# Optimization experiments

Hardware: AMD Instinct MI355X
Metric: run time of the kernel (lower is better)

Reference implementation:

```python
import jax, jax.numpy as jnp
import numpy as np

IN_F = 1024
OUT_F = 1024
DEGREE = 7  # degree+1 = 8 Chebyshev terms


def setup_inputs() -> dict:
    key = jax.random.key(0)
    k1, k2, k3 = jax.random.split(key, 3)
    x = jax.random.normal(k1, (16384, IN_F), dtype=jnp.float32)
    std = 1.0 / (IN_F * (DEGREE + 1))
    cheby_coeffs = jax.random.normal(k2, (OUT_F, IN_F, DEGREE + 1), dtype=jnp.float32) * std
    # xavier_uniform for base_weight [out, in]
    limit = float(np.sqrt(6.0 / (IN_F + OUT_F)))
    base_weight = jax.random.uniform(k3, (OUT_F, IN_F), dtype=jnp.float32, minval=-limit, maxval=limit)
    return {"x": x, "cheby_coeffs": cheby_coeffs, "base_weight": base_weight}


def _cheby_basis(x_norm, degree):
    terms = [jnp.ones_like(x_norm), x_norm]
    for _ in range(2, degree + 1):
        terms.append(2.0 * x_norm * terms[-1] - terms[-2])
    return jnp.stack(terms, axis=-1)  # [b, i, d+1]


def reference(x, cheby_coeffs, base_weight):
    x_norm = jnp.tanh(x)
    basis = _cheby_basis(x_norm, DEGREE)               # [b, i, d]
    kan_out = jnp.einsum('bid,oid->bo', basis, cheby_coeffs)
    base_out = x @ base_weight.T                        # F.linear
    return kan_out + base_out
```

## Files before the change

### kernel.cpp

```cpp
#include <hip/hip_runtime.h>
#include <hip/hip_bf16.h>
#include <stdint.h>

typedef short short8 __attribute__((ext_vector_type(8)));
typedef float f32x16 __attribute__((ext_vector_type(16)));

#define KD 8192
#define NT 128

__device__ __forceinline__ unsigned short bfb(float f) {
    __hip_bfloat16 h = __float2bfloat16(f);
    return __builtin_bit_cast(unsigned short, h);
}

__device__ __forceinline__ short8 cheby8(float xv) {
    float e  = __builtin_amdgcn_exp2f(xv * 2.8853900817779268f);
    float xn = 1.0f - 2.0f * __builtin_amdgcn_rcpf(1.0f + e);
    float x2 = xn + xn;
    float t2 = x2 * xn - 1.0f;
    float t3 = x2 * t2 - xn;
    float t4 = x2 * t3 - t2;
    float t5 = x2 * t4 - t3;
    float t6 = x2 * t5 - t4;
    float t7 = x2 * t6 - t5;
    short8 v;
    v[0] = bfb(xv); v[1] = bfb(xn); v[2] = bfb(t2); v[3] = bfb(t3);
    v[4] = bfb(t4); v[5] = bfb(t5); v[6] = bfb(t6); v[7] = bfb(t7);
    return v;
}

__global__ void prep_w(const float* __restrict__ C, const float* __restrict__ W,
                       unsigned short* __restrict__ Bw) {
    int g = blockIdx.x * 256 + threadIdx.x;
    int o = g >> 10, i = g & 1023;
    const float* src = C + ((size_t)o * 8192 + i * 8);
    float4 v0 = *(const float4*)src;
    float4 v1 = *(const float4*)(src + 4);
    v0.x = W[o * 1024 + i];
    short8 r;
    r[0] = bfb(v0.x); r[1] = bfb(v0.y); r[2] = bfb(v0.z); r[3] = bfb(v0.w);
    r[4] = bfb(v1.x); r[5] = bfb(v1.y); r[6] = bfb(v1.z); r[7] = bfb(v1.w);
    *(short8*)(Bw + (size_t)g * 8) = r;
}

__global__ void prep_bias(const float* __restrict__ C, float* __restrict__ bias) {
    int o = blockIdx.x;
    int tid = threadIdx.x;
    float s = 0.f;
    for (int i = tid; i < 1024; i += 256)
        s += C[(size_t)o * 8192 + (size_t)i * 8];
    #pragma unroll
    for (int off = 32; off > 0; off >>= 1) s += __shfl_down(s, off);
    __shared__ float red[4];
    if ((tid & 63) == 0) red[tid >> 6] = s;
    __syncthreads();
    if (tid == 0) bias[o] = red[0] + red[1] + red[2] + red[3];
}


#define GLDS(NXT_, C_, TT_) \
    __builtin_amdgcn_global_load_lds( \
        (const __attribute__((address_space(1))) unsigned int*)((const char*)Bw + boff[C_] + (size_t)(TT_) * 128), \
        (__attribute__((address_space(3))) unsigned int*)(&Bs[NXT_][(wave * 4 + (C_)) * 8][0]), 16, 0, 0)

#define PHASE(CUR_, KK_) { \
    const int fb_ = (KK_) * 2 + lg;   \
    float xv0_ = Xs[CUR_][fb_][wm + lr]; \
    float xv1_ = Xs[CUR_][fb_][wm + 32 + lr]; \
    float xv2_ = Xs[CUR_][fb_][wm + 64 + lr]; \
    float xv3_ = Xs[CUR_][fb_][wm + 96 + lr]; \
    const int row0_ = wn + lr, row1_ = wn + 32 + lr; \
    short8 b0_ = *(const short8*)((const char*)&Bs[CUR_][0][0] + row0_ * 128 + ((fb_ ^ (row0_ & 7)) * 16)); \
    short8 b1_ = *(const short8*)((const char*)&Bs[CUR_][0][0] + row1_ * 128 + ((fb_ ^ (row1_ & 7)) * 16)); \
    short8 a0_ = cheby8(xv0_); \
    short8 a1_ = cheby8(xv1_); \
    short8 a2_ = cheby8(xv2_); \
    short8 a3_ = cheby8(xv3_); \
    __builtin_amdgcn_s_setprio(1); \
    acc[0][0] = __builtin_amdgcn_mfma_f32_32x32x16_bf16(a0_, b0_, acc[0][0], 0, 0, 0); \
    acc[0][1] = __builtin_amdgcn_mfma_f32_32x32x16_bf16(a0_, b1_, acc[0][1], 0, 0, 0); \
    acc[1][0] = __builtin_amdgcn_mfma_f32_32x32x16_bf16(a1_, b0_, acc[1][0], 0, 0, 0); \
    acc[1][1] = __builtin_amdgcn_mfma_f32_32x32x16_bf16(a1_, b1_, acc[1][1], 0, 0, 0); \
    acc[2][0] = __builtin_amdgcn_mfma_f32_32x32x16_bf16(a2_, b0_, acc[2][0], 0, 0, 0); \
    acc[2][1] = __builtin_amdgcn_mfma_f32_32x32x16_bf16(a2_, b1_, acc[2][1], 0, 0, 0); \
    acc[3][0] = __builtin_amdgcn_mfma_f32_32x32x16_bf16(a3_, b0_, acc[3][0], 0, 0, 0); \
    acc[3][1] = __builtin_amdgcn_mfma_f32_32x32x16_bf16(a3_, b1_, acc[3][1], 0, 0, 0); \
    __builtin_amdgcn_s_setprio(0); \
}

#define TILE(CUR_, NXT_, T_) { \
    const int tn_ = ((T_) + 1 < NT) ? (T_) + 1 : NT - 1; \
    float4 xr_ = *(const float4*)(xbase + (size_t)tn_ * 8);   \
    GLDS(NXT_, 0, tn_); GLDS(NXT_, 1, tn_); GLDS(NXT_, 2, tn_); GLDS(NXT_, 3, tn_); \
    PHASE(CUR_, 0) \
    PHASE(CUR_, 1) \
    Xs[NXT_][xf + 0][arow] = xr_.x; \
    Xs[NXT_][xf + 1][arow] = xr_.y; \
    Xs[NXT_][xf + 2][arow] = xr_.z; \
    Xs[NXT_][xf + 3][arow] = xr_.w; \
    PHASE(CUR_, 2) \
    PHASE(CUR_, 3) \
    __syncthreads(); \
}

__global__ __launch_bounds__(512, 2)
void cheby_gemm(const float* __restrict__ X, const unsigned short* __restrict__ Bw,
                const float* __restrict__ bias, float* __restrict__ Out) {
    __shared__ unsigned short Bs[2][256][64];
    __shared__ float Xs[2][8][256];

    const int tid  = threadIdx.x;
    const int lane = tid & 63;
    const int wave = tid >> 6;

    int bid = blockIdx.x;
    int lin = (bid & 7) * 32 + (bid >> 3);
    const int m0 = (lin & 63) << 8;
    const int n0 = (lin >> 6) << 8;

    const int wm = (wave >> 2) * 128;
    const int wn = (wave & 3) * 64;
    const int lr = lane & 31;
    const int lg = lane >> 5;

    const int arow = tid >> 1;
    const int xf   = (tid & 1) * 4;
    const float* xbase = X + (size_t)(m0 + arow) * 1024 + xf;

    unsigned int boff[4];
    #pragma unroll
    for (int c = 0; c < 4; ++c) {
        int row   = (wave * 4 + c) * 8 + (lane >> 3);
        int chunk = (lane & 7) ^ (lane >> 3);
        boff[c] = ((unsigned)(n0 + row) * 8192u + (unsigned)chunk * 8u) * 2u;
    }

    f32x16 acc[4][2] = {};

    {
        float4 xr_ = *(const float4*)(xbase);
        GLDS(0, 0, 0); GLDS(0, 1, 0); GLDS(0, 2, 0); GLDS(0, 3, 0);
        Xs[0][xf + 0][arow] = xr_.x;
        Xs[0][xf + 1][arow] = xr_.y;
        Xs[0][xf + 2][arow] = xr_.z;
        Xs[0][xf + 3][arow] = xr_.w;
        __syncthreads();
    }

    for (int t = 0; t < NT; t += 2) {
        TILE(0, 1, t)
        TILE(1, 0, t + 1)
    }

    #pragma unroll
    for (int ni = 0; ni < 2; ++ni) {
        int col = n0 + wn + ni * 32 + lr;
        float bv = bias[col];
        #pragma unroll
        for (int mi = 0; mi < 4; ++mi) {
            #pragma unroll
            for (int r = 0; r < 16; ++r) {
                int row = m0 + wm + mi * 32 + 4 * lg + (r & 3) + 8 * (r >> 2);
                Out[(size_t)row * 1024 + col] = acc[mi][ni][r] + bv;
            }
        }
    }
}

extern "C" void kernel_launch(void* const* d_in, const int* in_sizes, int n_in,
                              void* d_out, int out_size, void* d_ws, size_t ws_size,
                              hipStream_t stream) {
    const float* x = (const float*)d_in[0];
    const float* C = (const float*)d_in[1];
    const float* W = (const float*)d_in[2];
    float* out = (float*)d_out;

    unsigned short* Bw = (unsigned short*)d_ws;
    float* bias = (float*)((char*)d_ws + (size_t)16 * 1024 * 1024);

    prep_w<<<4096, 256, 0, stream>>>(C, W, Bw);
    prep_bias<<<1024, 256, 0, stream>>>(C, bias);
    cheby_gemm<<<256, 512, 0, stream>>>(x, Bw, bias, out);
}
```

Baseline: 321.0 us.

## Reshape wave tile to 64x128 and hand-schedule loads with explicit waitcnts

Each wave now covers 64 rows by 128 columns instead of 128 by 64. That halves how often the Chebyshev basis (exp, rcp, recurrence, bf16 conversions) is recomputed for each x element across waves. The cost is twice as many B-fragment LDS reads per phase. The X global load moves to inline asm, and `__syncthreads` is replaced by explicit `s_waitcnt vmcnt`/`lgkmcnt` plus `s_barrier` with sched_barriers, so global_load_lds of the next tile can overlap the four MFMA phases. The X store to LDS now happens after all phases. The hand-written vmcnt counts risk being wrong if the compiler emits extra memory operations.

```diff
diff --git a/kernel.cpp b/kernel.cpp
--- a/kernel.cpp
+++ b/kernel.cpp
@@ -63,44 +63,54 @@
         (const __attribute__((address_space(1))) unsigned int*)((const char*)Bw + boff[C_] + (size_t)(TT_) * 128), \
         (__attribute__((address_space(3))) unsigned int*)(&Bs[NXT_][(wave * 4 + (C_)) * 8][0]), 16, 0, 0)
 
+#define XLOAD(DST_, TI_) { \
+    const float* ap_ = xbase + (size_t)(TI_) * 8; \
+    asm volatile("global_load_dwordx4 %0, %1, off" : "=&v"(DST_) : "v"(ap_)); }
+
 #define PHASE(CUR_, KK_) { \
-    const int fb_ = (KK_) * 2 + lg;   \
+    const int fb_ = (KK_) * 2 + lg; \
+    const int co_ = (fb_ ^ (lr & 7)) * 16; \
     float xv0_ = Xs[CUR_][fb_][wm + lr]; \
     float xv1_ = Xs[CUR_][fb_][wm + 32 + lr]; \
-    float xv2_ = Xs[CUR_][fb_][wm + 64 + lr]; \
-    float xv3_ = Xs[CUR_][fb_][wm + 96 + lr]; \
-    const int row0_ = wn + lr, row1_ = wn + 32 + lr; \
-    short8 b0_ = *(const short8*)((const char*)&Bs[CUR_][0][0] + row0_ * 128 + ((fb_ ^ (row0_ & 7)) * 16)); \
-    short8 b1_ = *(const short8*)((const char*)&Bs[CUR_][0][0] + row1_ * 128 + ((fb_ ^ (row1_ & 7)) * 16)); \
+    short8 b0_ = *(const short8*)((const char*)&Bs[CUR_][0][0] + (wn +  0 + lr) * 128 + co_); \
+    short8 b1_ = *(const short8*)((const char*)&Bs[CUR_][0][0] + (wn + 32 + lr) * 128 + co_); \
+    short8 b2_ = *(const short8*)((const char*)&Bs[CUR_][0][0] + (wn + 64 + lr) * 128 + co_); \
+    short8 b3_ = *(const short8*)((const char*)&Bs[CUR_][0][0] + (wn + 96 + lr) * 128 + co_); \
     short8 a0_ = cheby8(xv0_); \
     short8 a1_ = cheby8(xv1_); \
-    short8 a2_ = cheby8(xv2_); \
-    short8 a3_ = cheby8(xv3_); \
     __builtin_amdgcn_s_setprio(1); \
     acc[0][0] = __builtin_amdgcn_mfma_f32_32x32x16_bf16(a0_, b0_, acc[0][0], 0, 0, 0); \
     acc[0][1] = __builtin_amdgcn_mfma_f32_32x32x16_bf16(a0_, b1_, acc[0][1], 0, 0, 0); \
+    acc[0][2] = __builtin_amdgcn_mfma_f32_32x32x16_bf16(a0_, b2_, acc[0][2], 0, 0, 0); \
+    acc[0][3] = __builtin_amdgcn_mfma_f32_32x32x16_bf16(a0_, b3_, acc[0][3], 0, 0, 0); \
     acc[1][0] = __builtin_amdgcn_mfma_f32_32x32x16_bf16(a1_, b0_, acc[1][0], 0, 0, 0); \
     acc[1][1] = __builtin_amdgcn_mfma_f32_32x32x16_bf16(a1_, b1_, acc[1][1], 0, 0, 0); \
-    acc[2][0] = __builtin_amdgcn_mfma_f32_32x32x16_bf16(a2_, b0_, acc[2][0], 0, 0, 0); \
-    acc[2][1] = __builtin_amdgcn_mfma_f32_32x32x16_bf16(a2_, b1_, acc[2][1], 0, 0, 0); \
-    acc[3][0] = __builtin_amdgcn_mfma_f32_32x32x16_bf16(a3_, b0_, acc[3][0], 0, 0, 0); \
-    acc[3][1] = __builtin_amdgcn_mfma_f32_32x32x16_bf16(a3_, b1_, acc[3][1], 0, 0, 0); \
+    acc[1][2] = __builtin_amdgcn_mfma_f32_32x32x16_bf16(a1_, b2_, acc[1][2], 0, 0, 0); \
+    acc[1][3] = __builtin_amdgcn_mfma_f32_32x32x16_bf16(a1_, b3_, acc[1][3], 0, 0, 0); \
     __builtin_amdgcn_s_setprio(0); \
 }
 
 #define TILE(CUR_, NXT_, T_) { \
     const int tn_ = ((T_) + 1 < NT) ? (T_) + 1 : NT - 1; \
-    float4 xr_ = *(const float4*)(xbase + (size_t)tn_ * 8);   \
+    float4 xr_; \
+    XLOAD(xr_, tn_) \
     GLDS(NXT_, 0, tn_); GLDS(NXT_, 1, tn_); GLDS(NXT_, 2, tn_); GLDS(NXT_, 3, tn_); \
+    asm volatile("s_waitcnt vmcnt(5)" ::: "memory");  \
+    __builtin_amdgcn_sched_barrier(0); \
+    __builtin_amdgcn_s_barrier(); \
     PHASE(CUR_, 0) \
     PHASE(CUR_, 1) \
+    PHASE(CUR_, 2) \
+    PHASE(CUR_, 3) \
+    asm volatile("s_waitcnt vmcnt(4)" ::: "memory");  \
+    __builtin_amdgcn_sched_barrier(0); \
     Xs[NXT_][xf + 0][arow] = xr_.x; \
     Xs[NXT_][xf + 1][arow] = xr_.y; \
     Xs[NXT_][xf + 2][arow] = xr_.z; \
     Xs[NXT_][xf + 3][arow] = xr_.w; \
-    PHASE(CUR_, 2) \
-    PHASE(CUR_, 3) \
-    __syncthreads(); \
+    asm volatile("s_waitcnt lgkmcnt(0)" ::: "memory"); \
+    __builtin_amdgcn_sched_barrier(0); \
+    __builtin_amdgcn_s_barrier(); \
 }
 
 __global__ __launch_bounds__(512, 2)
@@ -118,8 +128,8 @@
     const int m0 = (lin & 63) << 8;
     const int n0 = (lin >> 6) << 8;
 
-    const int wm = (wave >> 2) * 128;
-    const int wn = (wave & 3) * 64;
+    const int wm = (wave >> 1) * 64;
+    const int wn = (wave & 1) * 128;
     const int lr = lane & 31;
     const int lg = lane >> 5;
 
@@ -135,16 +145,21 @@
         boff[c] = ((unsigned)(n0 + row) * 8192u + (unsigned)chunk * 8u) * 2u;
     }
 
-    f32x16 acc[4][2] = {};
+    f32x16 acc[2][4] = {};
 
     {
-        float4 xr_ = *(const float4*)(xbase);
+        float4 xr_;
+        XLOAD(xr_, 0)
         GLDS(0, 0, 0); GLDS(0, 1, 0); GLDS(0, 2, 0); GLDS(0, 3, 0);
+        asm volatile("s_waitcnt vmcnt(4)" ::: "memory");
+        __builtin_amdgcn_sched_barrier(0);
         Xs[0][xf + 0][arow] = xr_.x;
         Xs[0][xf + 1][arow] = xr_.y;
         Xs[0][xf + 2][arow] = xr_.z;
         Xs[0][xf + 3][arow] = xr_.w;
-        __syncthreads();
+        asm volatile("s_waitcnt lgkmcnt(0)" ::: "memory");
+        __builtin_amdgcn_sched_barrier(0);
+        __builtin_amdgcn_s_barrier();
     }
 
     for (int t = 0; t < NT; t += 2) {
@@ -153,11 +168,11 @@
     }
 
     #pragma unroll
-    for (int ni = 0; ni < 2; ++ni) {
+    for (int ni = 0; ni < 4; ++ni) {
         int col = n0 + wn + ni * 32 + lr;
         float bv = bias[col];
         #pragma unroll
-        for (int mi = 0; mi < 4; ++mi) {
+        for (int mi = 0; mi < 2; ++mi) {
             #pragma unroll
             for (int r = 0; r < 16; ++r) {
                 int row = m0 + wm + mi * 32 + 4 * lg + (r & 3) + 8 * (r >> 2);
```

Result: faster. 282.8 us (-11.9%).
